# Optimization experiments

Measured on AMD Instinct MI355X. Metric: run time of the kernel, lower is better.

Reference implementation:

```python
import jax, jax.numpy as jnp
import numpy as np

N = 50000    # nodes
P = 4        # meta-paths
E = 800000   # edges per meta-path (avg degree 16)
IN = 256     # in_size
OUT = 128    # out_size


def _xavier(key, shape, gain=1.0):
    fan_in, fan_out = shape[-2], shape[-1]
    lim = gain * np.sqrt(6.0 / (fan_in + fan_out))
    return jax.random.uniform(key, shape, jnp.float32, -lim, lim)


def setup_inputs() -> dict:
    key = jax.random.key(0)
    ks = jax.random.split(key, 8)
    x = jax.random.normal(ks[0], (N, IN), jnp.float32)
    src = jax.random.randint(ks[1], (P, E), 0, N)
    dst = jax.random.randint(ks[2], (P, E), 0, N)
    # per-meta-path GraphConv weight/bias (dgl default: xavier weight, zero bias)
    W = _xavier(ks[3], (P, IN, OUT))
    b_conv = jnp.zeros((P, OUT), jnp.float32)
    # semantic attention vectors, xavier with gain=1.414 on shape (1, OUT)
    att_lim = 1.414 * np.sqrt(6.0 / (1 + OUT))
    att = jax.random.uniform(ks[4], (P, OUT), jnp.float32, -att_lim, att_lim)
    fc_w = _xavier(ks[5], (OUT, OUT))
    fc_b = jnp.zeros((OUT,), jnp.float32)
    h_bias = jnp.zeros((OUT,), jnp.float32)
    return {"x": x, "W": W, "b_conv": b_conv, "att": att,
            "fc_w": fc_w, "fc_b": fc_b, "h_bias": h_bias,
            "src": src, "dst": dst}


def _graphconv(x, src, dst, W, b):
    # dgl GraphConv, norm='both', allow_zero_in_degree=True (degrees clamped to 1)
    ones_e = jnp.ones(src.shape[0], x.dtype)
    deg_out = jnp.maximum(jax.ops.segment_sum(ones_e, src, num_segments=N), 1.0)
    deg_in = jnp.maximum(jax.ops.segment_sum(ones_e, dst, num_segments=N), 1.0)
    # weight applied before aggregation (in_size > out_size path) -- same math
    xw = (x * jax.lax.rsqrt(deg_out)[:, None]) @ W          # [N, OUT]
    agg = jax.ops.segment_sum(xw[src], dst, num_segments=N)  # [N, OUT]
    return agg * jax.lax.rsqrt(deg_in)[:, None] + b


def reference(x, W, b_conv, att, fc_w, fc_b, h_bias, src, dst):
    # one GraphConv per meta-path (P is a small fixed structural set)
    hs = [_graphconv(x, src[i], dst[i], W[i], b_conv[i]) for i in range(P)]
    # semantic attention: sp_i = tanh(fc(h_i)).mean(0); beta_i = att_i . sp_i
    sp = jnp.stack([jnp.tanh(h @ fc_w.T + fc_b).mean(axis=0) for h in hs])  # [P, OUT]
    beta = jax.nn.softmax(jnp.sum(att * sp, axis=-1))  # [P]
    h = hs[0] * beta[0]
    for i in range(1, P):
        h = h + hs[i] * beta[i]
    # epilogue: bias (self_loop=False, activation=None, dropout eval = identity)
    return h + h_bias
```

## Files before the change

kernel.cpp:

```cpp
#include <hip/hip_runtime.h>
#include <math.h>

#define N_NODES 50000
#define P_PATHS 4
#define E_EDGES 800000
#define IN_F 256
#define OUT_F 128
#define NPB 128
#define NBUCK 391
#define NCHUNK 200
#define CHUNK_E (E_EDGES / NCHUNK)
#define GBLK 391
#define DSL 20
#define QTR 4
#define Q_N 12500
#define Q_W 6250
#define AP 264
#define FP 136

typedef unsigned short ushort_t;
typedef unsigned int uint_t;
typedef float f32x4 __attribute__((ext_vector_type(4)));
typedef short s16x8 __attribute__((ext_vector_type(8)));

__device__ __forceinline__ ushort_t f2bf(float f) {
    uint_t u = __float_as_uint(f);
    return (ushort_t)((u + 0x7FFFu + ((u >> 16) & 1u)) >> 16);
}
__device__ __forceinline__ float bf2f(ushort_t h) {
    return __uint_as_float(((uint_t)h) << 16);
}

__global__ void prep_kernel(const float* __restrict__ W, const float* __restrict__ fcw,
                            ushort_t* __restrict__ Wt, ushort_t* __restrict__ fcwb)
{
    int idx = blockIdx.x * blockDim.x + threadIdx.x;
    if (idx < P_PATHS * IN_F * OUT_F) {
        int p = idx >> 15;
        int r = idx & 32767;
        int k = r >> 7;
        int n = r & 127;
        Wt[((size_t)p << 15) + (size_t)n * IN_F + k] = f2bf(W[idx]);
    }
    if (idx < OUT_F * OUT_F) fcwb[idx] = f2bf(fcw[idx]);
}

__global__ __launch_bounds__(256) void deghist_kernel(const int* __restrict__ src,
                                                      uint_t* __restrict__ dhist)
{
    __shared__ uint_t cnt[Q_W];
    int sl = blockIdx.x, q = blockIdx.y, p = blockIdx.z;
    int t = threadIdx.x;
    int nbase = q * Q_N;
    for (int i = t; i < Q_W; i += 256) cnt[i] = 0;
    __syncthreads();
    const int4* s4 = (const int4*)(src + (size_t)p * E_EDGES + (size_t)sl * (E_EDGES / DSL));
    for (int i = t; i < E_EDGES / DSL / 4; i += 256) {
        int4 v = s4[i];
        uint_t r;
        r = (uint_t)(v.x - nbase); if (r < Q_N) atomicAdd(&cnt[r >> 1], 1u << ((r & 1) * 16));
        r = (uint_t)(v.y - nbase); if (r < Q_N) atomicAdd(&cnt[r >> 1], 1u << ((r & 1) * 16));
        r = (uint_t)(v.z - nbase); if (r < Q_N) atomicAdd(&cnt[r >> 1], 1u << ((r & 1) * 16));
        r = (uint_t)(v.w - nbase); if (r < Q_N) atomicAdd(&cnt[r >> 1], 1u << ((r & 1) * 16));
    }
    __syncthreads();
    uint_t* outp = dhist + (((size_t)p * QTR + q) * DSL + sl) * Q_W;
    for (int i = t; i < Q_W; i += 256) outp[i] = cnt[i];
}

__global__ void rsout_kernel(const uint_t* __restrict__ dhist, float* __restrict__ rsout)
{
    int idx = blockIdx.x * 256 + threadIdx.x;
    if (idx >= P_PATHS * QTR * Q_W) return;
    int ph = idx / Q_W;
    int w  = idx % Q_W;
    const uint_t* base = dhist + (size_t)ph * DSL * Q_W + w;
    uint_t s = 0;
#pragma unroll
    for (int sl = 0; sl < DSL; ++sl) s += base[(size_t)sl * Q_W];
    int p = ph >> 2, q = ph & 3;
    int node = q * Q_N + 2 * w;
    uint_t c0 = s & 0xFFFFu, c1 = s >> 16;
    rsout[(size_t)p * N_NODES + node]     = rsqrtf((float)(c0 ? c0 : 1u));
    rsout[(size_t)p * N_NODES + node + 1] = rsqrtf((float)(c1 ? c1 : 1u));
}

__global__ __launch_bounds__(256) void bhist_kernel(const int* __restrict__ dst,
                                                    uint_t* __restrict__ bcounts)
{
    __shared__ uint_t bh[NBUCK];
    int p = blockIdx.y;
    int t = threadIdx.x;
    for (int i = t; i < NBUCK; i += 256) bh[i] = 0;
    __syncthreads();
    const int4* d4 = (const int4*)(dst + (size_t)p * E_EDGES + (size_t)blockIdx.x * CHUNK_E);
    for (int i = t; i < CHUNK_E / 4; i += 256) {
        int4 v = d4[i];
        atomicAdd(&bh[v.x >> 7], 1u);
        atomicAdd(&bh[v.y >> 7], 1u);
        atomicAdd(&bh[v.z >> 7], 1u);
        atomicAdd(&bh[v.w >> 7], 1u);
    }
    __syncthreads();
    for (int i = t; i < NBUCK; i += 256)
        if (bh[i]) atomicAdd(&bcounts[p * NBUCK + i], bh[i]);
}

__global__ __launch_bounds__(1024) void bscan_kernel(const uint_t* __restrict__ bcounts,
                                                     int* __restrict__ bstart,
                                                     int* __restrict__ bcursor)
{
    __shared__ int a[2048], b[2048];
    int t = threadIdx.x;
    for (int i = t; i < 2048; i += 1024)
        a[i] = (i < P_PATHS * NBUCK) ? (int)bcounts[i] : 0;
    __syncthreads();
    int* pin = a; int* pout = b;
    for (int off = 1; off < 2048; off <<= 1) {
        for (int i = t; i < 2048; i += 1024)
            pout[i] = pin[i] + (i >= off ? pin[i - off] : 0);
        __syncthreads();
        int* tmp = pin; pin = pout; pout = tmp;
    }
    for (int i = t; i < P_PATHS * NBUCK; i += 1024) {
        int st = pin[i] - (int)bcounts[i];
        bstart[i] = st;
        bcursor[i] = st;
    }
    if (t == 0) bstart[P_PATHS * NBUCK] = pin[P_PATHS * NBUCK - 1];
}

__global__ __launch_bounds__(256) void bscatter_kernel(const int* __restrict__ src,
                                                       const int* __restrict__ dst,
                                                       int* __restrict__ bcursor,
                                                       uint_t* __restrict__ ebuf)
{
    __shared__ uint_t bh[NBUCK];
    __shared__ uint_t lbase[NBUCK];
    int p = blockIdx.y;
    int t = threadIdx.x;
    int sub = p * E_EDGES;
    int* bcursor_p = bcursor + p * NBUCK;
    uint_t* ebuf_p = ebuf + (size_t)p * E_EDGES;
    for (int i = t; i < NBUCK; i += 256) bh[i] = 0;
    __syncthreads();
    size_t ebase = (size_t)p * E_EDGES + (size_t)blockIdx.x * CHUNK_E;
    const int4* d4 = (const int4*)(dst + ebase);
    const int4* s4 = (const int4*)(src + ebase);
    for (int i = t; i < CHUNK_E / 4; i += 256) {
        int4 v = d4[i];
        atomicAdd(&bh[v.x >> 7], 1u);
        atomicAdd(&bh[v.y >> 7], 1u);
        atomicAdd(&bh[v.z >> 7], 1u);
        atomicAdd(&bh[v.w >> 7], 1u);
    }
    __syncthreads();
    for (int i = t; i < NBUCK; i += 256) {
        uint_t c = bh[i];
        lbase[i] = c ? (uint_t)(atomicAdd(&bcursor_p[i], (int)c) - sub) : 0u;
        bh[i] = 0;
    }
    __syncthreads();
    for (int i = t; i < CHUNK_E / 4; i += 256) {
        int4 d = d4[i];
        int4 s = s4[i];
        { int bk = d.x >> 7; uint_t pos = lbase[bk] + atomicAdd(&bh[bk], 1u); ebuf_p[pos] = (uint_t)s.x | ((uint_t)(d.x & 127) << 16); }
        { int bk = d.y >> 7; uint_t pos = lbase[bk] + atomicAdd(&bh[bk], 1u); ebuf_p[pos] = (uint_t)s.y | ((uint_t)(d.y & 127) << 16); }
        { int bk = d.z >> 7; uint_t pos = lbase[bk] + atomicAdd(&bh[bk], 1u); ebuf_p[pos] = (uint_t)s.z | ((uint_t)(d.z & 127) << 16); }
        { int bk = d.w >> 7; uint_t pos = lbase[bk] + atomicAdd(&bh[bk], 1u); ebuf_p[pos] = (uint_t)s.w | ((uint_t)(d.w & 127) << 16); }
    }
}

__global__ __launch_bounds__(256) void blocal_kernel(const uint_t* __restrict__ ebuf,
                                                     const int* __restrict__ bstart,
                                                     ushort_t* __restrict__ eidx2,
                                                     int* __restrict__ rsn)
{
    __shared__ uint_t hist[NPB];
    __shared__ uint_t cur[NPB];
    __shared__ uint_t sa[NPB], sb[NPB];
    int bkt = blockIdx.x;
    int p = blockIdx.y;
    int t = threadIdx.x;
    int sub = p * E_EDGES;
    const uint_t* ebuf_p = ebuf + (size_t)p * E_EDGES;
    ushort_t* eidx2_p = eidx2 + (size_t)p * E_EDGES;
    int* rsn_p = rsn + (size_t)p * (N_NODES + 1);
    if (t < NPB) hist[t] = 0;
    __syncthreads();
    int r0 = bstart[p * NBUCK + bkt] - sub;
    int r1 = bstart[p * NBUCK + bkt + 1] - sub;
    for (int e = r0 + t; e < r1; e += 256)
        atomicAdd(&hist[ebuf_p[e] >> 16], 1u);
    __syncthreads();
    if (t < NPB) sa[t] = hist[t];
    __syncthreads();
    uint_t* pin = sa; uint_t* pout = sb;
    for (int off = 1; off < NPB; off <<= 1) {
        if (t < NPB) pout[t] = pin[t] + (t >= off ? pin[t - off] : 0u);
        __syncthreads();
        uint_t* tmp = pin; pin = pout; pout = tmp;
    }
    if (t < NPB) {
        uint_t ex = pin[t] - hist[t];
        int node = bkt * NPB + t;
        if (node < N_NODES) rsn_p[node] = r0 + (int)ex;
        cur[t] = ex;
    }
    if (bkt == NBUCK - 1 && t == 0) rsn_p[N_NODES] = r1;
    __syncthreads();
    for (int e = r0 + t; e < r1; e += 256) {
        uint_t pk = ebuf_p[e];
        int dl = (int)(pk >> 16);
        uint_t pos = atomicAdd(&cur[dl], 1u);
        eidx2_p[r0 + pos] = (ushort_t)(pk & 0xFFFFu);
    }
}

__global__ __launch_bounds__(256) void gemm_xall_kernel(const float* __restrict__ x,
                                                        const ushort_t* __restrict__ Wt,
                                                        const float* __restrict__ rsout,
                                                        ushort_t* __restrict__ xwb)
{
    __shared__ ushort_t As[128 * AP];
    __shared__ ushort_t Bs[128 * AP];
    int m0 = blockIdx.x * 128;
    int t = threadIdx.x;
    int wid = t >> 6, lane = t & 63;
    int wr = wid >> 1, wc = wid & 1;
    int srow = t >> 1, half = (t & 1) * 16;
    int gr = m0 + srow;
#pragma unroll
    for (int c = 0; c < 8; ++c) {
        int kb = c * 32 + half;
        uint4 w0 = make_uint4(0, 0, 0, 0), w1 = make_uint4(0, 0, 0, 0);
        if (gr < N_NODES) {
            const float* ap = x + (size_t)gr * IN_F + kb;
            float4 f0 = *(const float4*)(ap + 0);
            float4 f1 = *(const float4*)(ap + 4);
            float4 f2 = *(const float4*)(ap + 8);
            float4 f3 = *(const float4*)(ap + 12);
            w0.x = (uint_t)f2bf(f0.x) | ((uint_t)f2bf(f0.y) << 16);
            w0.y = (uint_t)f2bf(f0.z) | ((uint_t)f2bf(f0.w) << 16);
            w0.z = (uint_t)f2bf(f1.x) | ((uint_t)f2bf(f1.y) << 16);
            w0.w = (uint_t)f2bf(f1.z) | ((uint_t)f2bf(f1.w) << 16);
            w1.x = (uint_t)f2bf(f2.x) | ((uint_t)f2bf(f2.y) << 16);
            w1.y = (uint_t)f2bf(f2.z) | ((uint_t)f2bf(f2.w) << 16);
            w1.z = (uint_t)f2bf(f3.x) | ((uint_t)f2bf(f3.y) << 16);
            w1.w = (uint_t)f2bf(f3.z) | ((uint_t)f2bf(f3.w) << 16);
        }
        *(uint4*)&As[srow * AP + kb]     = w0;
        *(uint4*)&As[srow * AP + kb + 8] = w1;
    }
    for (int p = 0; p < P_PATHS; ++p) {
        __syncthreads();
        const ushort_t* Wp = Wt + ((size_t)p << 15);
#pragma unroll
        for (int c = 0; c < 8; ++c) {
            int kb = c * 32 + half;
            const ushort_t* bp = Wp + (size_t)srow * IN_F + kb;
            *(uint4*)&Bs[srow * AP + kb]     = *(const uint4*)(bp);
            *(uint4*)&Bs[srow * AP + kb + 8] = *(const uint4*)(bp + 8);
        }
        __syncthreads();
        f32x4 acc[4][4] = {};
#pragma unroll
        for (int k0 = 0; k0 < IN_F; k0 += 32) {
            s16x8 aF[4], bF[4];
            int kk = k0 + (lane >> 4) * 8;
#pragma unroll
            for (int m = 0; m < 4; ++m)
                aF[m] = *(const s16x8*)&As[(wr * 64 + m * 16 + (lane & 15)) * AP + kk];
#pragma unroll
            for (int n = 0; n < 4; ++n)
                bF[n] = *(const s16x8*)&Bs[(wc * 64 + n * 16 + (lane & 15)) * AP + kk];
#pragma unroll
            for (int m = 0; m < 4; ++m)
#pragma unroll
                for (int n = 0; n < 4; ++n)
                    acc[m][n] = __builtin_amdgcn_mfma_f32_16x16x32_bf16(aF[m], bF[n], acc[m][n], 0, 0, 0);
        }
        ushort_t* xp = xwb + (size_t)p * N_NODES * OUT_F;
        const float* rp = rsout + (size_t)p * N_NODES;
#pragma unroll
        for (int m = 0; m < 4; ++m) {
#pragma unroll
            for (int i = 0; i < 4; ++i) {
                int row = m0 + wr * 64 + m * 16 + (lane >> 4) * 4 + i;
                if (row < N_NODES) {
                    float rs = rp[row];
#pragma unroll
                    for (int n = 0; n < 4; ++n) {
                        int col = wc * 64 + n * 16 + (lane & 15);
                        xp[(size_t)row * OUT_F + col] = f2bf(acc[m][n][i] * rs);
                    }
                }
            }
        }
    }
}

__global__ __launch_bounds__(256) void gather_kernel(const ushort_t* __restrict__ xwb,
                                                     const ushort_t* __restrict__ eidx2,
                                                     const int* __restrict__ rsn,
                                                     const float* __restrict__ bconv,
                                                     uint_t* __restrict__ hb)
{
    int wid = threadIdx.x >> 6, lane = threadIdx.x & 63;
    int p = blockIdx.y;
    int n = blockIdx.x * 4 + wid;
    const int* rsn_p = rsn + (size_t)p * (N_NODES + 1);
    const ushort_t* eidx2_p = eidx2 + (size_t)p * E_EDGES;
    int b = rsn_p[n], e = rsn_p[n + 1];
    const uint_t* base = (const uint_t*)xwb + (size_t)p * N_NODES * 64 + lane;
    float a0 = 0.f, a1 = 0.f;
    int i = b;
    for (; i + 3 < e; i += 4) {
        int s0 = eidx2_p[i], s1 = eidx2_p[i + 1], s2 = eidx2_p[i + 2], s3 = eidx2_p[i + 3];
        uint_t w0 = base[(size_t)s0 * 64];
        uint_t w1 = base[(size_t)s1 * 64];
        uint_t w2 = base[(size_t)s2 * 64];
        uint_t w3 = base[(size_t)s3 * 64];
        a0 += (bf2f((ushort_t)w0) + bf2f((ushort_t)w1)) + (bf2f((ushort_t)w2) + bf2f((ushort_t)w3));
        a1 += (bf2f((ushort_t)(w0 >> 16)) + bf2f((ushort_t)(w1 >> 16))) +
              (bf2f((ushort_t)(w2 >> 16)) + bf2f((ushort_t)(w3 >> 16)));
    }
    for (; i < e; ++i) {
        int s = eidx2_p[i];
        uint_t w = base[(size_t)s * 64];
        a0 += bf2f((ushort_t)w);
        a1 += bf2f((ushort_t)(w >> 16));
    }
    int d = e - b;
    float sc = rsqrtf((float)(d > 0 ? d : 1));
    float2 bc = *(const float2*)(bconv + (size_t)p * OUT_F + 2 * lane);
    float r0 = fmaf(a0, sc, bc.x);
    float r1 = fmaf(a1, sc, bc.y);
    hb[((size_t)p * N_NODES + n) * 64 + lane] = (uint_t)f2bf(r0) | ((uint_t)f2bf(r1) << 16);
}

__global__ __launch_bounds__(256) void fc_mfma_kernel(const ushort_t* __restrict__ hb,
                                                      const ushort_t* __restrict__ fcwb,
                                                      const float* __restrict__ fcb,
                                                      float* __restrict__ partial)
{
    __shared__ ushort_t As[128 * FP];
    __shared__ ushort_t Bs[128 * FP];
    __shared__ float red[2][128];
    int m0 = blockIdx.x * 128;
    int p = blockIdx.y;
    int t = threadIdx.x;
    int wid = t >> 6, lane = t & 63;
    int wr = wid >> 1, wc = wid & 1;
    int srow = t >> 1, half = (t & 1) * 16;
    int gr = m0 + srow;
    const ushort_t* hp = hb + (size_t)p * N_NODES * OUT_F;
#pragma unroll
    for (int c = 0; c < 4; ++c) {
        int kb = c * 32 + half;
        uint4 w0 = make_uint4(0, 0, 0, 0), w1 = make_uint4(0, 0, 0, 0);
        if (gr < N_NODES) {
            const ushort_t* ap = hp + (size_t)gr * OUT_F + kb;
            w0 = *(const uint4*)(ap);
            w1 = *(const uint4*)(ap + 8);
        }
        *(uint4*)&As[srow * FP + kb]     = w0;
        *(uint4*)&As[srow * FP + kb + 8] = w1;
        const ushort_t* bp = fcwb + (size_t)srow * OUT_F + kb;
        *(uint4*)&Bs[srow * FP + kb]     = *(const uint4*)(bp);
        *(uint4*)&Bs[srow * FP + kb + 8] = *(const uint4*)(bp + 8);
    }
    __syncthreads();
    f32x4 acc[4][4] = {};
#pragma unroll
    for (int k0 = 0; k0 < OUT_F; k0 += 32) {
        s16x8 aF[4], bF[4];
        int kk = k0 + (lane >> 4) * 8;
#pragma unroll
        for (int m = 0; m < 4; ++m)
            aF[m] = *(const s16x8*)&As[(wr * 64 + m * 16 + (lane & 15)) * FP + kk];
#pragma unroll
        for (int n = 0; n < 4; ++n)
            bF[n] = *(const s16x8*)&Bs[(wc * 64 + n * 16 + (lane & 15)) * FP + kk];
#pragma unroll
        for (int m = 0; m < 4; ++m)
#pragma unroll
            for (int n = 0; n < 4; ++n)
                acc[m][n] = __builtin_amdgcn_mfma_f32_16x16x32_bf16(aF[m], bF[n], acc[m][n], 0, 0, 0);
    }
#pragma unroll
    for (int n = 0; n < 4; ++n) {
        int col = wc * 64 + n * 16 + (lane & 15);
        float fb = fcb[col];
        float s = 0.f;
#pragma unroll
        for (int m = 0; m < 4; ++m)
#pragma unroll
            for (int i = 0; i < 4; ++i) {
                int row = m0 + wr * 64 + m * 16 + (lane >> 4) * 4 + i;
                if (row < N_NODES) s += tanhf(acc[m][n][i] + fb);
            }
        s += __shfl_xor(s, 16);
        s += __shfl_xor(s, 32);
        if (lane < 16) red[wr][col] = s;
    }
    __syncthreads();
    if (t < 128)
        partial[((size_t)p * GBLK + blockIdx.x) * OUT_F + t] = red[0][t] + red[1][t];
}

__global__ __launch_bounds__(512) void beta_reduce_kernel(const float* __restrict__ partial,
                                                          const float* __restrict__ att,
                                                          float* __restrict__ beta)
{
    int t = threadIdx.x;
    int p = t >> 7, c = t & 127;
    float s = 0.f;
    for (int i = 0; i < GBLK; ++i)
        s += partial[((size_t)p * GBLK + i) * OUT_F + c];
    float v = att[p * OUT_F + c] * (s * (1.0f / N_NODES));
    __shared__ float red[512];
    red[t] = v;
    __syncthreads();
    for (int off = 64; off >= 1; off >>= 1) {
        if (c < off) red[t] += red[t + off];
        __syncthreads();
    }
    if (t == 0) {
        float w[P_PATHS], mx = -1e30f;
        for (int q = 0; q < P_PATHS; ++q) { w[q] = red[q * 128]; mx = fmaxf(mx, w[q]); }
        float sum = 0.f;
        for (int q = 0; q < P_PATHS; ++q) { w[q] = expf(w[q] - mx); sum += w[q]; }
        for (int q = 0; q < P_PATHS; ++q) beta[q] = w[q] / sum;
    }
}

__global__ void combine_kernel(const uint_t* __restrict__ hb, const float* __restrict__ hbias,
                               const float* __restrict__ beta, float* __restrict__ out)
{
    int idx = blockIdx.x * blockDim.x + threadIdx.x;
    if (idx >= N_NODES * 64) return;
    int n = idx >> 6;
    int w = idx & 63;
    float2 hbv = *(const float2*)(hbias + 2 * w);
    float r0 = hbv.x, r1 = hbv.y;
#pragma unroll
    for (int p = 0; p < P_PATHS; ++p) {
        float bp = beta[p];
        uint_t v = hb[((size_t)p * N_NODES + n) * 64 + w];
        r0 = fmaf(bp, bf2f((ushort_t)v), r0);
        r1 = fmaf(bp, bf2f((ushort_t)(v >> 16)), r1);
    }
    *(float2*)(out + (size_t)n * OUT_F + 2 * w) = make_float2(r0, r1);
}

extern "C" void kernel_launch(void* const* d_in, const int* in_sizes, int n_in,
                              void* d_out, int out_size, void* d_ws, size_t ws_size,
                              hipStream_t stream)
{
    const float* x      = (const float*)d_in[0];
    const float* W      = (const float*)d_in[1];
    const float* b_conv = (const float*)d_in[2];
    const float* att    = (const float*)d_in[3];
    const float* fc_w   = (const float*)d_in[4];
    const float* fc_b   = (const float*)d_in[5];
    const float* h_bias = (const float*)d_in[6];
    const int*   src    = (const int*)d_in[7];
    const int*   dst    = (const int*)d_in[8];
    float* out = (float*)d_out;
    float* ws  = (float*)d_ws;

    size_t off_rsout   = 0;
    size_t off_partial = off_rsout + (size_t)P_PATHS * N_NODES;
    size_t off_beta    = off_partial + (size_t)P_PATHS * GBLK * OUT_F;
    size_t off_i32     = (off_beta + 4 + 63) & ~(size_t)63;
    size_t i_bstart  = 0;
    size_t i_bcursor = 1600;
    size_t i_bcounts = 3200;
    size_t i_rsn     = 4800;
    size_t i_dhist   = 204864;
    size_t i_ebuf    = i_dhist + (size_t)P_PATHS * QTR * DSL * Q_W;
    size_t n_ints    = i_ebuf + (size_t)P_PATHS * E_EDGES;
    size_t off_u16   = off_i32 + ((n_ints + 63) & ~(size_t)63);
    size_t u_hb    = 0;
    size_t u_xwb   = u_hb + (size_t)P_PATHS * N_NODES * OUT_F;
    size_t u_eidx2 = u_xwb + (size_t)P_PATHS * N_NODES * OUT_F;
    size_t u_Wt    = u_eidx2 + (size_t)P_PATHS * E_EDGES;
    size_t u_fcwb  = u_Wt + (size_t)P_PATHS * IN_F * OUT_F;

    float* rsout   = ws + off_rsout;
    float* partial = ws + off_partial;
    float* beta    = ws + off_beta;
    int*   ibase   = (int*)(ws + off_i32);
    int*    bstart  = ibase + i_bstart;
    int*    bcursor = ibase + i_bcursor;
    uint_t* bcounts = (uint_t*)(ibase + i_bcounts);
    int*    rsn     = ibase + i_rsn;
    uint_t* dhist   = (uint_t*)(ibase + i_dhist);
    uint_t* ebuf    = (uint_t*)(ibase + i_ebuf);
    ushort_t* ubase = (ushort_t*)(ws + off_u16);
    ushort_t* hb    = ubase + u_hb;
    ushort_t* xwb   = ubase + u_xwb;
    ushort_t* eidx2 = ubase + u_eidx2;
    ushort_t* Wt    = ubase + u_Wt;
    ushort_t* fcwb  = ubase + u_fcwb;

    hipMemsetAsync(bcounts, 0, (size_t)P_PATHS * NBUCK * sizeof(uint_t), stream);

    prep_kernel<<<(P_PATHS * IN_F * OUT_F + 255) / 256, 256, 0, stream>>>(W, fc_w, Wt, fcwb);
    deghist_kernel<<<dim3(DSL, QTR, P_PATHS), 256, 0, stream>>>(src, dhist);
    rsout_kernel<<<(P_PATHS * QTR * Q_W + 255) / 256, 256, 0, stream>>>(dhist, rsout);
    bhist_kernel<<<dim3(NCHUNK, P_PATHS), 256, 0, stream>>>(dst, bcounts);
    bscan_kernel<<<1, 1024, 0, stream>>>(bcounts, bstart, bcursor);

    gemm_xall_kernel<<<GBLK, 256, 0, stream>>>(x, Wt, rsout, xwb);
    bscatter_kernel<<<dim3(NCHUNK, P_PATHS), 256, 0, stream>>>(src, dst, bcursor, ebuf);
    blocal_kernel<<<dim3(NBUCK, P_PATHS), 256, 0, stream>>>(ebuf, bstart, eidx2, rsn);
    gather_kernel<<<dim3(N_NODES / 4, P_PATHS), 256, 0, stream>>>(
        xwb, eidx2, rsn, b_conv, (uint_t*)hb);
    fc_mfma_kernel<<<dim3(GBLK, P_PATHS), 256, 0, stream>>>(hb, fcwb, fc_b, partial);

    beta_reduce_kernel<<<1, 512, 0, stream>>>(partial, att, beta);
    combine_kernel<<<(N_NODES * 64 + 255) / 256, 256, 0, stream>>>(
        (const uint_t*)hb, h_bias, beta, out);
}
```

Baseline: 361.7 us.

## Merge histogram/scan launches, split GEMM over paths, gather two nodes per wave

Folds the destination bucket histogram into the degree-histogram launch as an extra grid slice, and folds the bucket scan into the rsout launch as an extra block. This removes two kernel launches. The x@W GEMM grid now splits the four meta-paths across two y-blocks, doubling the block count at the cost of converting the x tile twice. The gather kernel now has each wave process two destination nodes with interleaved loads, giving more memory-level parallelism per wave from more in-flight gathers, at the cost of extra registers.

```diff
diff --git a/kernel.cpp b/kernel.cpp
--- a/kernel.cpp
+++ b/kernel.cpp
@@ -17,6 +17,7 @@
 #define Q_W 6250
 #define AP 264
 #define FP 136
+#define RSB 196
 
 typedef unsigned short ushort_t;
 typedef unsigned int uint_t;
@@ -46,11 +47,29 @@
 }
 
 __global__ __launch_bounds__(256) void deghist_kernel(const int* __restrict__ src,
-                                                      uint_t* __restrict__ dhist)
+                                                      const int* __restrict__ dst,
+                                                      uint_t* __restrict__ dhist,
+                                                      uint_t* __restrict__ bcounts)
 {
     __shared__ uint_t cnt[Q_W];
     int sl = blockIdx.x, q = blockIdx.y, p = blockIdx.z;
     int t = threadIdx.x;
+    if (q == QTR) {
+        for (int i = t; i < NBUCK; i += 256) cnt[i] = 0;
+        __syncthreads();
+        const int4* d4 = (const int4*)(dst + (size_t)p * E_EDGES + (size_t)sl * (E_EDGES / DSL));
+        for (int i = t; i < E_EDGES / DSL / 4; i += 256) {
+            int4 v = d4[i];
+            atomicAdd(&cnt[v.x >> 7], 1u);
+            atomicAdd(&cnt[v.y >> 7], 1u);
+            atomicAdd(&cnt[v.z >> 7], 1u);
+            atomicAdd(&cnt[v.w >> 7], 1u);
+        }
+        __syncthreads();
+        for (int i = t; i < NBUCK; i += 256)
+            if (cnt[i]) atomicAdd(&bcounts[p * NBUCK + i], cnt[i]);
+        return;
+    }
     int nbase = q * Q_N;
     for (int i = t; i < Q_W; i += 256) cnt[i] = 0;
     __syncthreads();
@@ -68,9 +87,34 @@
     for (int i = t; i < Q_W; i += 256) outp[i] = cnt[i];
 }
 
-__global__ void rsout_kernel(const uint_t* __restrict__ dhist, float* __restrict__ rsout)
-{
-    int idx = blockIdx.x * 256 + threadIdx.x;
+__global__ __launch_bounds__(1024) void rsout_bscan_kernel(const uint_t* __restrict__ dhist,
+                                                           float* __restrict__ rsout,
+                                                           const uint_t* __restrict__ bcounts,
+                                                           int* __restrict__ bstart,
+                                                           int* __restrict__ bcursor)
+{
+    int t = threadIdx.x;
+    if (blockIdx.x == RSB) {
+        __shared__ int a[2048], b[2048];
+        for (int i = t; i < 2048; i += 1024)
+            a[i] = (i < P_PATHS * NBUCK) ? (int)bcounts[i] : 0;
+        __syncthreads();
+        int* pin = a; int* pout = b;
+        for (int off = 1; off < 2048; off <<= 1) {
+            for (int i = t; i < 2048; i += 1024)
+                pout[i] = pin[i] + (i >= off ? pin[i - off] : 0);
+            __syncthreads();
+            int* tmp = pin; pin = pout; pout = tmp;
+        }
+        for (int i = t; i < P_PATHS * NBUCK; i += 1024) {
+            int st = pin[i] - (int)bcounts[i];
+            bstart[i] = st;
+            bcursor[i] = st;
+        }
+        if (t == 0) bstart[P_PATHS * NBUCK] = pin[P_PATHS * NBUCK - 1];
+        return;
+    }
+    int idx = blockIdx.x * 1024 + t;
     if (idx >= P_PATHS * QTR * Q_W) return;
     int ph = idx / Q_W;
     int w  = idx % Q_W;
@@ -83,51 +127,6 @@
     uint_t c0 = s & 0xFFFFu, c1 = s >> 16;
     rsout[(size_t)p * N_NODES + node]     = rsqrtf((float)(c0 ? c0 : 1u));
     rsout[(size_t)p * N_NODES + node + 1] = rsqrtf((float)(c1 ? c1 : 1u));
-}
-
-__global__ __launch_bounds__(256) void bhist_kernel(const int* __restrict__ dst,
-                                                    uint_t* __restrict__ bcounts)
-{
-    __shared__ uint_t bh[NBUCK];
-    int p = blockIdx.y;
-    int t = threadIdx.x;
-    for (int i = t; i < NBUCK; i += 256) bh[i] = 0;
-    __syncthreads();
-    const int4* d4 = (const int4*)(dst + (size_t)p * E_EDGES + (size_t)blockIdx.x * CHUNK_E);
-    for (int i = t; i < CHUNK_E / 4; i += 256) {
-        int4 v = d4[i];
-        atomicAdd(&bh[v.x >> 7], 1u);
-        atomicAdd(&bh[v.y >> 7], 1u);
-        atomicAdd(&bh[v.z >> 7], 1u);
-        atomicAdd(&bh[v.w >> 7], 1u);
-    }
-    __syncthreads();
-    for (int i = t; i < NBUCK; i += 256)
-        if (bh[i]) atomicAdd(&bcounts[p * NBUCK + i], bh[i]);
-}
-
-__global__ __launch_bounds__(1024) void bscan_kernel(const uint_t* __restrict__ bcounts,
-                                                     int* __restrict__ bstart,
-                                                     int* __restrict__ bcursor)
-{
-    __shared__ int a[2048], b[2048];
-    int t = threadIdx.x;
-    for (int i = t; i < 2048; i += 1024)
-        a[i] = (i < P_PATHS * NBUCK) ? (int)bcounts[i] : 0;
-    __syncthreads();
-    int* pin = a; int* pout = b;
-    for (int off = 1; off < 2048; off <<= 1) {
-        for (int i = t; i < 2048; i += 1024)
-            pout[i] = pin[i] + (i >= off ? pin[i - off] : 0);
-        __syncthreads();
-        int* tmp = pin; pin = pout; pout = tmp;
-    }
-    for (int i = t; i < P_PATHS * NBUCK; i += 1024) {
-        int st = pin[i] - (int)bcounts[i];
-        bstart[i] = st;
-        bcursor[i] = st;
-    }
-    if (t == 0) bstart[P_PATHS * NBUCK] = pin[P_PATHS * NBUCK - 1];
 }
 
 __global__ __launch_bounds__(256) void bscatter_kernel(const int* __restrict__ src,
@@ -252,7 +251,8 @@
         *(uint4*)&As[srow * AP + kb]     = w0;
         *(uint4*)&As[srow * AP + kb + 8] = w1;
     }
-    for (int p = 0; p < P_PATHS; ++p) {
+    for (int pp = 0; pp < 2; ++pp) {
+        int p = blockIdx.y * 2 + pp;
         __syncthreads();
         const ushort_t* Wp = Wt + ((size_t)p << 15);
 #pragma unroll
@@ -308,15 +308,34 @@
 {
     int wid = threadIdx.x >> 6, lane = threadIdx.x & 63;
     int p = blockIdx.y;
-    int n = blockIdx.x * 4 + wid;
+    int n0 = (blockIdx.x * 4 + wid) * 2;
     const int* rsn_p = rsn + (size_t)p * (N_NODES + 1);
     const ushort_t* eidx2_p = eidx2 + (size_t)p * E_EDGES;
-    int b = rsn_p[n], e = rsn_p[n + 1];
+    int bA = rsn_p[n0], mid = rsn_p[n0 + 1], eB = rsn_p[n0 + 2];
     const uint_t* base = (const uint_t*)xwb + (size_t)p * N_NODES * 64 + lane;
-    float a0 = 0.f, a1 = 0.f;
-    int i = b;
-    for (; i + 3 < e; i += 4) {
-        int s0 = eidx2_p[i], s1 = eidx2_p[i + 1], s2 = eidx2_p[i + 2], s3 = eidx2_p[i + 3];
+    float a0 = 0.f, a1 = 0.f, b0 = 0.f, b1 = 0.f;
+    int iA = bA, iB = mid;
+    while (iA + 4 <= mid && iB + 4 <= eB) {
+        int sA0 = eidx2_p[iA], sA1 = eidx2_p[iA + 1], sA2 = eidx2_p[iA + 2], sA3 = eidx2_p[iA + 3];
+        int sB0 = eidx2_p[iB], sB1 = eidx2_p[iB + 1], sB2 = eidx2_p[iB + 2], sB3 = eidx2_p[iB + 3];
+        uint_t wA0 = base[(size_t)sA0 * 64];
+        uint_t wA1 = base[(size_t)sA1 * 64];
+        uint_t wA2 = base[(size_t)sA2 * 64];
+        uint_t wA3 = base[(size_t)sA3 * 64];
+        uint_t wB0 = base[(size_t)sB0 * 64];
+        uint_t wB1 = base[(size_t)sB1 * 64];
+        uint_t wB2 = base[(size_t)sB2 * 64];
+        uint_t wB3 = base[(size_t)sB3 * 64];
+        a0 += (bf2f((ushort_t)wA0) + bf2f((ushort_t)wA1)) + (bf2f((ushort_t)wA2) + bf2f((ushort_t)wA3));
+        a1 += (bf2f((ushort_t)(wA0 >> 16)) + bf2f((ushort_t)(wA1 >> 16))) +
+              (bf2f((ushort_t)(wA2 >> 16)) + bf2f((ushort_t)(wA3 >> 16)));
+        b0 += (bf2f((ushort_t)wB0) + bf2f((ushort_t)wB1)) + (bf2f((ushort_t)wB2) + bf2f((ushort_t)wB3));
+        b1 += (bf2f((ushort_t)(wB0 >> 16)) + bf2f((ushort_t)(wB1 >> 16))) +
+              (bf2f((ushort_t)(wB2 >> 16)) + bf2f((ushort_t)(wB3 >> 16)));
+        iA += 4; iB += 4;
+    }
+    for (; iA + 4 <= mid; iA += 4) {
+        int s0 = eidx2_p[iA], s1 = eidx2_p[iA + 1], s2 = eidx2_p[iA + 2], s3 = eidx2_p[iA + 3];
         uint_t w0 = base[(size_t)s0 * 64];
         uint_t w1 = base[(size_t)s1 * 64];
         uint_t w2 = base[(size_t)s2 * 64];
@@ -325,18 +344,34 @@
         a1 += (bf2f((ushort_t)(w0 >> 16)) + bf2f((ushort_t)(w1 >> 16))) +
               (bf2f((ushort_t)(w2 >> 16)) + bf2f((ushort_t)(w3 >> 16)));
     }
-    for (; i < e; ++i) {
-        int s = eidx2_p[i];
-        uint_t w = base[(size_t)s * 64];
+    for (; iA < mid; ++iA) {
+        uint_t w = base[(size_t)eidx2_p[iA] * 64];
         a0 += bf2f((ushort_t)w);
         a1 += bf2f((ushort_t)(w >> 16));
     }
-    int d = e - b;
-    float sc = rsqrtf((float)(d > 0 ? d : 1));
+    for (; iB + 4 <= eB; iB += 4) {
+        int s0 = eidx2_p[iB], s1 = eidx2_p[iB + 1], s2 = eidx2_p[iB + 2], s3 = eidx2_p[iB + 3];
+        uint_t w0 = base[(size_t)s0 * 64];
+        uint_t w1 = base[(size_t)s1 * 64];
+        uint_t w2 = base[(size_t)s2 * 64];
+        uint_t w3 = base[(size_t)s3 * 64];
+        b0 += (bf2f((ushort_t)w0) + bf2f((ushort_t)w1)) + (bf2f((ushort_t)w2) + bf2f((ushort_t)w3));
+        b1 += (bf2f((ushort_t)(w0 >> 16)) + bf2f((ushort_t)(w1 >> 16))) +
+              (bf2f((ushort_t)(w2 >> 16)) + bf2f((ushort_t)(w3 >> 16)));
+    }
+    for (; iB < eB; ++iB) {
+        uint_t w = base[(size_t)eidx2_p[iB] * 64];
+        b0 += bf2f((ushort_t)w);
+        b1 += bf2f((ushort_t)(w >> 16));
+    }
+    int dA = mid - bA, dB = eB - mid;
+    float scA = rsqrtf((float)(dA > 0 ? dA : 1));
+    float scB = rsqrtf((float)(dB > 0 ? dB : 1));
     float2 bc = *(const float2*)(bconv + (size_t)p * OUT_F + 2 * lane);
-    float r0 = fmaf(a0, sc, bc.x);
-    float r1 = fmaf(a1, sc, bc.y);
-    hb[((size_t)p * N_NODES + n) * 64 + lane] = (uint_t)f2bf(r0) | ((uint_t)f2bf(r1) << 16);
+    hb[((size_t)p * N_NODES + n0) * 64 + lane] =
+        (uint_t)f2bf(fmaf(a0, scA, bc.x)) | ((uint_t)f2bf(fmaf(a1, scA, bc.y)) << 16);
+    hb[((size_t)p * N_NODES + n0 + 1) * 64 + lane] =
+        (uint_t)f2bf(fmaf(b0, scB, bc.x)) | ((uint_t)f2bf(fmaf(b1, scB, bc.y)) << 16);
 }
 
 __global__ __launch_bounds__(256) void fc_mfma_kernel(const ushort_t* __restrict__ hb,
@@ -508,15 +543,13 @@
     hipMemsetAsync(bcounts, 0, (size_t)P_PATHS * NBUCK * sizeof(uint_t), stream);
 
     prep_kernel<<<(P_PATHS * IN_F * OUT_F + 255) / 256, 256, 0, stream>>>(W, fc_w, Wt, fcwb);
-    deghist_kernel<<<dim3(DSL, QTR, P_PATHS), 256, 0, stream>>>(src, dhist);
-    rsout_kernel<<<(P_PATHS * QTR * Q_W + 255) / 256, 256, 0, stream>>>(dhist, rsout);
-    bhist_kernel<<<dim3(NCHUNK, P_PATHS), 256, 0, stream>>>(dst, bcounts);
-    bscan_kernel<<<1, 1024, 0, stream>>>(bcounts, bstart, bcursor);
-
-    gemm_xall_kernel<<<GBLK, 256, 0, stream>>>(x, Wt, rsout, xwb);
+    deghist_kernel<<<dim3(DSL, QTR + 1, P_PATHS), 256, 0, stream>>>(src, dst, dhist, bcounts);
+    rsout_bscan_kernel<<<RSB + 1, 1024, 0, stream>>>(dhist, rsout, bcounts, bstart, bcursor);
+
+    gemm_xall_kernel<<<dim3(GBLK, 2), 256, 0, stream>>>(x, Wt, rsout, xwb);
     bscatter_kernel<<<dim3(NCHUNK, P_PATHS), 256, 0, stream>>>(src, dst, bcursor, ebuf);
     blocal_kernel<<<dim3(NBUCK, P_PATHS), 256, 0, stream>>>(ebuf, bstart, eidx2, rsn);
-    gather_kernel<<<dim3(N_NODES / 4, P_PATHS), 256, 0, stream>>>(
+    gather_kernel<<<dim3(N_NODES / 8, P_PATHS), 256, 0, stream>>>(
         xwb, eidx2, rsn, b_conv, (uint_t*)hb);
     fc_mfma_kernel<<<dim3(GBLK, P_PATHS), 256, 0, stream>>>(hb, fcwb, fc_b, partial);
 
```

Result: faster. 331.2 us (-8.4%).
